# Optimization experiments

Measured on AMD Instinct MI355X. Metric: run time of the kernel, lower is better.

Reference implementation:

```python
import jax, jax.numpy as jnp
import numpy as np

M = 7          # init kwarg m
TAU = 3        # init kwarg tau
C_IN = 7       # init kwarg c_in
KSIZE = M + 1  # 8
NUM_KERNELS = 74
PAD = M * TAU  # 21, left-pad only
RAND_CH = 0    # original uses torch.randint at forward time; fixed for determinism


def setup_inputs() -> dict:
    key = jax.random.key(0)
    k1, k2 = jax.random.split(key)
    x = jax.random.normal(k1, (32, 8192, C_IN), dtype=jnp.float32)
    # learned parameter: self.kernels, shape [num_kernels, kernel_size]
    kernels = jax.random.normal(k2, (NUM_KERNELS, KSIZE), dtype=jnp.float32)
    return {"x": x, "kernels": kernels}


def reference(x, kernels):
    B, S, C = x.shape
    # pad left with zeros on time axis: [B, C, S+PAD]
    xp = jnp.pad(jnp.transpose(x, (0, 2, 1)), ((0, 0), (0, 0), (PAD, 0)))
    W = (S + PAD - KSIZE) // TAU + 1  # number of unfolded windows
    idx = jnp.arange(W)[:, None] * TAU + jnp.arange(KSIZE)[None, :]  # [W, K]
    windows = xp[:, :, idx]  # [B, C, W, K]
    # The 73-iteration depthwise conv1d loop (each output length 1) is exactly a
    # dot product of each window with each kernel. torch.cat over the loop is
    # kernel-major in the channel dim -> layout [B, W, n, C] -> [B, W, n*C].
    main = jnp.einsum('bcwk,nk->bwnc', windows, kernels[:NUM_KERNELS - 1])
    main = main.reshape(B, W, (NUM_KERNELS - 1) * C)
    # final feature: one selected channel convolved with the last kernel
    final = jnp.einsum('bwk,k->bw', windows[:, RAND_CH], kernels[-1])[..., None]
    combined = jnp.concatenate([main, final], axis=2)  # [B, W, 73*C+1]
    return jnp.transpose(combined, (0, 2, 1))[:, :, :S]
```

## Files before the change

kernel.cpp:

```cpp
#include <hip/hip_runtime.h>


constexpr int Bn    = 32;
constexpr int Sn    = 8192;
constexpr int Cn    = 7;
constexpr int Kn    = 8;
constexpr int NKn   = 74;
constexpr int PADn  = 21;
constexpr int Wn    = 2736;
constexpr int OCH   = 512;
constexpr int WTILE = 256;
constexpr int NGROUP = 4;
constexpr int NSAMP = (WTILE - 1) * 3 + Kn;
constexpr int XTILE = NSAMP * Cn;

__global__ __launch_bounds__(256)
void strided_conv_kernel(const float* __restrict__ x,
                         const float* __restrict__ kern,
                         float* __restrict__ out) {
    __shared__ float lx[XTILE];
    __shared__ float lk[NKn * Kn];

    const int tid = threadIdx.x;
    const int w0  = blockIdx.x * WTILE;
    const int b   = blockIdx.y;
    const int g   = blockIdx.z;

    const int sbase7 = (w0 * 3 - PADn) * Cn;
    const float* xb = x + (size_t)b * (Sn * Cn);
    for (int i = tid; i < XTILE; i += 256) {
        int off = sbase7 + i;
        lx[i] = (off >= 0 && off < Sn * Cn) ? xb[off] : 0.0f;
    }
    for (int i = tid; i < NKn * Kn; i += 256) lk[i] = kern[i];
    __syncthreads();

    const int w = w0 + tid;
    if (w >= Wn) return;

    float win[Cn][Kn];
#pragma unroll
    for (int k = 0; k < Kn; ++k) {
        const int base = (tid * 3 + k) * Cn;
#pragma unroll
        for (int c = 0; c < Cn; ++c) win[c][k] = lx[base + c];
    }

    const int n0 = (73 * g) / NGROUP;
    const int n1 = (73 * (g + 1)) / NGROUP;
    float* ob = out + (size_t)b * OCH * Wn + w;

    for (int n = n0; n < n1; ++n) {
        float kn[Kn];
#pragma unroll
        for (int k = 0; k < Kn; ++k) kn[k] = lk[n * Kn + k];
#pragma unroll
        for (int c = 0; c < Cn; ++c) {
            float acc = 0.0f;
#pragma unroll
            for (int k = 0; k < Kn; ++k) acc = fmaf(win[c][k], kn[k], acc);
            ob[(size_t)(n * 7 + c) * Wn] = acc;
        }
    }
    if (g == NGROUP - 1) {
        float acc = 0.0f;
#pragma unroll
        for (int k = 0; k < Kn; ++k) acc = fmaf(win[0][k], lk[73 * Kn + k], acc);
        ob[(size_t)511 * Wn] = acc;
    }
}

extern "C" void kernel_launch(void* const* d_in, const int* in_sizes, int n_in,
                              void* d_out, int out_size, void* d_ws, size_t ws_size,
                              hipStream_t stream) {
    const float* x    = (const float*)d_in[0];
    const float* kern = (const float*)d_in[1];
    float* out        = (float*)d_out;

    dim3 grid((Wn + WTILE - 1) / WTILE, Bn, NGROUP);
    dim3 block(256);
    strided_conv_kernel<<<grid, block, 0, stream>>>(x, kern, out);
}
```

Measured before the change: 40.82 us.

## Split into transpose-pad prepass and vectorized conv with 4-wide output stores

Adds a prepass that transposes x to channel-major with left zero padding in workspace. The main kernel then loads contiguous 16-wide windows with vector loads, computes four consecutive windows per thread for four kernels, and writes float4 nontemporal stores. This targets uncoalesced scalar stores and the shared-memory staging of the old kernel. The cost is an extra launch and an extra pass over x through global memory, and the original kernel is kept as a fallback when workspace is too small.

```diff
diff --git a/kernel.cpp b/kernel.cpp
--- a/kernel.cpp
+++ b/kernel.cpp
@@ -1,43 +1,134 @@
 #include <hip/hip_runtime.h>
 
 
-constexpr int Bn    = 32;
-constexpr int Sn    = 8192;
-constexpr int Cn    = 7;
-constexpr int Kn    = 8;
-constexpr int NKn   = 74;
-constexpr int PADn  = 21;
-constexpr int Wn    = 2736;
-constexpr int OCH   = 512;
-constexpr int WTILE = 256;
-constexpr int NGROUP = 4;
-constexpr int NSAMP = (WTILE - 1) * 3 + Kn;
-constexpr int XTILE = NSAMP * Cn;
+typedef float f32x4 __attribute__((ext_vector_type(4)));
+
+constexpr int Bn   = 32;
+constexpr int Sn   = 8192;
+constexpr int Cn   = 7;
+constexpr int Kn   = 8;
+constexpr int PADn = 21;
+constexpr int Wn   = 2736;
+constexpr int OCH  = 512;
+constexpr int W4   = Wn / 4;
+constexpr int WQ   = W4 / 4;
+constexpr int XSTR = 8224;
+constexpr size_t XT_BYTES = (size_t)Bn * Cn * XSTR * 4;
 
 __global__ __launch_bounds__(256)
-void strided_conv_kernel(const float* __restrict__ x,
-                         const float* __restrict__ kern,
-                         float* __restrict__ out) {
+void transpose_pad(const float* __restrict__ x, float* __restrict__ xT) {
+    int idx = blockIdx.x * 256 + threadIdx.x;
+    const int total = Bn * Cn * XSTR;
+    if (idx >= total) return;
+    int s2  = idx % XSTR;
+    int rem = idx / XSTR;
+    int c   = rem % Cn;
+    int b   = rem / Cn;
+    int s   = s2 - PADn;
+    float v = 0.0f;
+    if (s >= 0 && s < Sn) v = x[((size_t)b * Sn + s) * Cn + c];
+    xT[idx] = v;
+}
+
+__global__ __launch_bounds__(256)
+void conv_main(const float* __restrict__ xT, const float* __restrict__ kern,
+               float* __restrict__ out) {
+    const int tid = threadIdx.x;
+    const int wq  = blockIdx.x;
+    const int g   = blockIdx.y;
+    const int b   = blockIdx.z;
+    const int n0  = 4 * g;
+    const bool last = (g == 18);
+
+    float kw[4][8];
+#pragma unroll
+    for (int j = 0; j < 4; ++j) {
+        if (j == 0 || !last) {
+            const float* kr = kern + (n0 + j) * Kn;
+#pragma unroll
+            for (int k = 0; k < 8; ++k) kw[j][k] = kr[k];
+        }
+    }
+    float kfin[8];
+    if (last) {
+#pragma unroll
+        for (int k = 0; k < 8; ++k) kfin[k] = kern[73 * Kn + k];
+    }
+
+    const float* xb = xT + (size_t)b * Cn * XSTR;
+    float* ob       = out + (size_t)b * OCH * Wn;
+
+    for (int s = tid; s < Cn * WQ; s += 256) {
+        int c   = s / WQ;
+        int w4  = wq * WQ + (s - c * WQ);
+        const float* xr = xb + c * XSTR + 12 * w4;
+
+        float xw[17];
+        *reinterpret_cast<f32x4*>(xw + 0)  = *reinterpret_cast<const f32x4*>(xr + 0);
+        *reinterpret_cast<f32x4*>(xw + 4)  = *reinterpret_cast<const f32x4*>(xr + 4);
+        *reinterpret_cast<f32x4*>(xw + 8)  = *reinterpret_cast<const f32x4*>(xr + 8);
+        *reinterpret_cast<f32x4*>(xw + 12) = *reinterpret_cast<const f32x4*>(xr + 12);
+        xw[16] = xr[16];
+
+#pragma unroll
+        for (int j = 0; j < 4; ++j) {
+            if (j == 0 || !last) {
+                float a0 = 0.f, a1 = 0.f, a2 = 0.f, a3 = 0.f;
+#pragma unroll
+                for (int k = 0; k < 8; ++k) {
+                    a0 = fmaf(xw[0 + k], kw[j][k], a0);
+                    a1 = fmaf(xw[3 + k], kw[j][k], a1);
+                    a2 = fmaf(xw[6 + k], kw[j][k], a2);
+                    a3 = fmaf(xw[9 + k], kw[j][k], a3);
+                }
+                f32x4 o = {a0, a1, a2, a3};
+                f32x4* dst = reinterpret_cast<f32x4*>(
+                    ob + (size_t)((n0 + j) * 7 + c) * Wn + 4 * w4);
+                __builtin_nontemporal_store(o, dst);
+            }
+        }
+        if (last && c == 0) {
+            float a0 = 0.f, a1 = 0.f, a2 = 0.f, a3 = 0.f;
+#pragma unroll
+            for (int k = 0; k < 8; ++k) {
+                a0 = fmaf(xw[0 + k], kfin[k], a0);
+                a1 = fmaf(xw[3 + k], kfin[k], a1);
+                a2 = fmaf(xw[6 + k], kfin[k], a2);
+                a3 = fmaf(xw[9 + k], kfin[k], a3);
+            }
+            f32x4 o = {a0, a1, a2, a3};
+            f32x4* dst = reinterpret_cast<f32x4*>(
+                ob + (size_t)511 * Wn + 4 * w4);
+            __builtin_nontemporal_store(o, dst);
+        }
+    }
+}
+
+constexpr int WTILE  = 256;
+constexpr int NGROUP = 4;
+constexpr int NSAMP  = (WTILE - 1) * 3 + Kn;
+constexpr int XTILE  = NSAMP * Cn;
+
+__global__ __launch_bounds__(256)
+void strided_conv_fallback(const float* __restrict__ x,
+                           const float* __restrict__ kern,
+                           float* __restrict__ out) {
     __shared__ float lx[XTILE];
-    __shared__ float lk[NKn * Kn];
-
+    __shared__ float lk[74 * Kn];
     const int tid = threadIdx.x;
     const int w0  = blockIdx.x * WTILE;
     const int b   = blockIdx.y;
     const int g   = blockIdx.z;
-
     const int sbase7 = (w0 * 3 - PADn) * Cn;
     const float* xb = x + (size_t)b * (Sn * Cn);
     for (int i = tid; i < XTILE; i += 256) {
         int off = sbase7 + i;
         lx[i] = (off >= 0 && off < Sn * Cn) ? xb[off] : 0.0f;
     }
-    for (int i = tid; i < NKn * Kn; i += 256) lk[i] = kern[i];
+    for (int i = tid; i < 74 * Kn; i += 256) lk[i] = kern[i];
     __syncthreads();
-
     const int w = w0 + tid;
     if (w >= Wn) return;
-
     float win[Cn][Kn];
 #pragma unroll
     for (int k = 0; k < Kn; ++k) {
@@ -45,11 +136,9 @@
 #pragma unroll
         for (int c = 0; c < Cn; ++c) win[c][k] = lx[base + c];
     }
-
     const int n0 = (73 * g) / NGROUP;
     const int n1 = (73 * (g + 1)) / NGROUP;
     float* ob = out + (size_t)b * OCH * Wn + w;
-
     for (int n = n0; n < n1; ++n) {
         float kn[Kn];
 #pragma unroll
@@ -77,7 +166,13 @@
     const float* kern = (const float*)d_in[1];
     float* out        = (float*)d_out;
 
-    dim3 grid((Wn + WTILE - 1) / WTILE, Bn, NGROUP);
-    dim3 block(256);
-    strided_conv_kernel<<<grid, block, 0, stream>>>(x, kern, out);
+    if (ws_size >= XT_BYTES) {
+        float* xT = (float*)d_ws;
+        const int total = Bn * Cn * XSTR;
+        transpose_pad<<<(total + 255) / 256, 256, 0, stream>>>(x, xT);
+        conv_main<<<dim3(4, 19, 32), 256, 0, stream>>>(xT, kern, out);
+    } else {
+        strided_conv_fallback<<<dim3((Wn + WTILE - 1) / WTILE, Bn, NGROUP),
+                                256, 0, stream>>>(x, kern, out);
+    }
 }
```

Measured after the change: 67.79 us. +66.1%, slower.

## Compute four windows per thread with float4 stores and channel-major padded LDS

Applied to the files above, without the earlier changes.

Each thread now computes four consecutive output windows per kernel and channel, sharing a 17-sample register window, and writes them with one 16-byte vector store instead of four scalar stores. The shared tile is transposed to channel-major with padding every 12 samples to avoid bank conflicts. Kernel rows are read directly from global memory, and each wavefront takes a strided subset of the kernels. This cuts store instruction count and LDS traffic but lowers thread-level parallelism, since there are fewer threads per output.

```diff
diff --git a/kernel.cpp b/kernel.cpp
--- a/kernel.cpp
+++ b/kernel.cpp
@@ -1,72 +1,87 @@
 #include <hip/hip_runtime.h>
 
 
-constexpr int Bn    = 32;
-constexpr int Sn    = 8192;
-constexpr int Cn    = 7;
-constexpr int Kn    = 8;
-constexpr int NKn   = 74;
-constexpr int PADn  = 21;
-constexpr int Wn    = 2736;
-constexpr int OCH   = 512;
-constexpr int WTILE = 256;
-constexpr int NGROUP = 4;
-constexpr int NSAMP = (WTILE - 1) * 3 + Kn;
-constexpr int XTILE = NSAMP * Cn;
+typedef float f32x4 __attribute__((ext_vector_type(4)));
+
+constexpr int Bn   = 32;
+constexpr int Sn   = 8192;
+constexpr int Cn   = 7;
+constexpr int Kn   = 8;
+constexpr int PADn = 21;
+constexpr int Wn   = 2736;
+constexpr int OCH  = 512;
+constexpr int NCH  = 684;
+constexpr int CHT  = 64;
+constexpr int NWQ  = 11;
+constexpr int SAMP = 773;
+constexpr int CSTR = 840;
 
 __global__ __launch_bounds__(256)
-void strided_conv_kernel(const float* __restrict__ x,
-                         const float* __restrict__ kern,
-                         float* __restrict__ out) {
-    __shared__ float lx[XTILE];
-    __shared__ float lk[NKn * Kn];
+void conv_v4(const float* __restrict__ x, const float* __restrict__ kern,
+             float* __restrict__ out) {
+    __shared__ float lx[Cn * CSTR];
 
     const int tid = threadIdx.x;
-    const int w0  = blockIdx.x * WTILE;
-    const int b   = blockIdx.y;
-    const int g   = blockIdx.z;
+    const int wq  = blockIdx.x;
+    const int g   = blockIdx.y;
+    const int b   = blockIdx.z;
 
-    const int sbase7 = (w0 * 3 - PADn) * Cn;
-    const float* xb = x + (size_t)b * (Sn * Cn);
-    for (int i = tid; i < XTILE; i += 256) {
-        int off = sbase7 + i;
-        lx[i] = (off >= 0 && off < Sn * Cn) ? xb[off] : 0.0f;
+    const int sbase = wq * 768 - PADn;
+    const int g0    = sbase * Cn;
+    const float* xb = x + (size_t)b * Sn * Cn;
+    for (int i = tid; i < SAMP * Cn; i += 256) {
+        int gg = g0 + i;
+        float v = (gg >= 0 && gg < Sn * Cn) ? xb[gg] : 0.0f;
+        int s = i / 7;
+        int c = i - 7 * s;
+        lx[c * CSTR + s + s / 12] = v;
     }
-    for (int i = tid; i < NKn * Kn; i += 256) lk[i] = kern[i];
     __syncthreads();
 
-    const int w = w0 + tid;
-    if (w >= Wn) return;
+    const int lane  = tid & 63;
+    const int r     = __builtin_amdgcn_readfirstlane(tid >> 6);
+    const int chunk = wq * CHT + lane;
+    if (chunk >= NCH) return;
 
-    float win[Cn][Kn];
+    const int n0 = (73 * g) / 4;
+    const int n1 = (73 * (g + 1)) / 4;
+    float* ob = out + (size_t)b * OCH * Wn + 4 * chunk;
+    const int base = 13 * lane;
+
+    for (int c = 0; c < Cn; ++c) {
+        float xw[17];
+        const float* lr = lx + c * CSTR + base;
 #pragma unroll
-    for (int k = 0; k < Kn; ++k) {
-        const int base = (tid * 3 + k) * Cn;
+        for (int j = 0; j < 17; ++j) xw[j] = lr[j + (j >= 12 ? 1 : 0)];
+
+        for (int n = n0 + r; n < n1; n += 4) {
+            const float* kr = kern + n * Kn;
+            float a0 = 0.f, a1 = 0.f, a2 = 0.f, a3 = 0.f;
 #pragma unroll
-        for (int c = 0; c < Cn; ++c) win[c][k] = lx[base + c];
-    }
-
-    const int n0 = (73 * g) / NGROUP;
-    const int n1 = (73 * (g + 1)) / NGROUP;
-    float* ob = out + (size_t)b * OCH * Wn + w;
-
-    for (int n = n0; n < n1; ++n) {
-        float kn[Kn];
+            for (int k = 0; k < 8; ++k) {
+                float kv = kr[k];
+                a0 = fmaf(xw[0 + k], kv, a0);
+                a1 = fmaf(xw[3 + k], kv, a1);
+                a2 = fmaf(xw[6 + k], kv, a2);
+                a3 = fmaf(xw[9 + k], kv, a3);
+            }
+            f32x4 o = {a0, a1, a2, a3};
+            *reinterpret_cast<f32x4*>(ob + (size_t)(n * 7 + c) * Wn) = o;
+        }
+        if (c == 0 && g == 3 && r == 3) {
+            const float* kr = kern + 73 * Kn;
+            float a0 = 0.f, a1 = 0.f, a2 = 0.f, a3 = 0.f;
 #pragma unroll
-        for (int k = 0; k < Kn; ++k) kn[k] = lk[n * Kn + k];
-#pragma unroll
-        for (int c = 0; c < Cn; ++c) {
-            float acc = 0.0f;
-#pragma unroll
-            for (int k = 0; k < Kn; ++k) acc = fmaf(win[c][k], kn[k], acc);
-            ob[(size_t)(n * 7 + c) * Wn] = acc;
+            for (int k = 0; k < 8; ++k) {
+                float kv = kr[k];
+                a0 = fmaf(xw[0 + k], kv, a0);
+                a1 = fmaf(xw[3 + k], kv, a1);
+                a2 = fmaf(xw[6 + k], kv, a2);
+                a3 = fmaf(xw[9 + k], kv, a3);
+            }
+            f32x4 o = {a0, a1, a2, a3};
+            *reinterpret_cast<f32x4*>(ob + (size_t)511 * Wn) = o;
         }
-    }
-    if (g == NGROUP - 1) {
-        float acc = 0.0f;
-#pragma unroll
-        for (int k = 0; k < Kn; ++k) acc = fmaf(win[0][k], lk[73 * Kn + k], acc);
-        ob[(size_t)511 * Wn] = acc;
     }
 }
 
@@ -77,7 +92,5 @@
     const float* kern = (const float*)d_in[1];
     float* out        = (float*)d_out;
 
-    dim3 grid((Wn + WTILE - 1) / WTILE, Bn, NGROUP);
-    dim3 block(256);
-    strided_conv_kernel<<<grid, block, 0, stream>>>(x, kern, out);
+    conv_v4<<<dim3(NWQ, 4, Bn), 256, 0, stream>>>(x, kern, out);
 }
```

Measured after the change: 40.43 us. About the same (-1.0%).
